# Performance work log

Measured on AMD Instinct MI355X. Metric: run time of the kernel, lower is better.

## Reference

```python
import jax, jax.numpy as jnp
import numpy as np

TOP_K = 8
SCORE_FUNC = "sigmoid"
ROUTE_NORM = True
ROUTE_SCALE = 2.5


def setup_inputs() -> dict:
    key = jax.random.key(0)
    k1, k2, k3 = jax.random.split(key, 3)
    B, S, H, E = 4, 4096, 2048, 64
    hidden_states = jax.random.normal(k1, (B, S, H), dtype=jnp.float32)
    # nn.Linear default init scale ~ 1/sqrt(H); exact distribution irrelevant for correctness
    gate_w = jax.random.normal(k2, (E, H), dtype=jnp.float32) * (1.0 / np.sqrt(H))
    expert_bias = jax.random.normal(k3, (E,), dtype=jnp.float32) * 0.1
    return {"hidden_states": hidden_states, "expert_bias": expert_bias, "gate_w": gate_w}


def reference(hidden_states, expert_bias, gate_w):
    B, S, H = hidden_states.shape
    x = hidden_states.reshape(-1, H)  # [T, H]
    logits = jnp.einsum("th,eh->te", x, gate_w)  # [T, E]
    if SCORE_FUNC == "sigmoid":
        scores = jax.nn.sigmoid(logits.astype(jnp.float32))
    else:
        scores = jax.nn.softmax(logits.astype(jnp.float32), axis=-1)
    if expert_bias is not None:
        _, selected_experts = jax.lax.top_k(scores + expert_bias[None, :], TOP_K)
        top_scores = jnp.take_along_axis(scores, selected_experts, axis=1)
    else:
        top_scores, selected_experts = jax.lax.top_k(scores, TOP_K)
    if SCORE_FUNC == "sigmoid" and ROUTE_NORM:
        denom = jnp.sum(top_scores, axis=-1, keepdims=True) + 1e-20
        top_scores = top_scores / denom
    top_scores = top_scores * ROUTE_SCALE
    return top_scores, selected_experts
```

## Files before the change

kernel.cpp:

```cpp
#include <hip/hip_runtime.h>
#include <math.h>

#define T_TOTAL 16384
#define HDIM    2048
#define NEXP    64
#define KS_MAIN 8

typedef unsigned short ushort_t;
using bf16x8 = __attribute__((ext_vector_type(8))) short;
using f32x4  = __attribute__((ext_vector_type(4))) float;

__device__ __forceinline__ unsigned bf16rne(float f) {
    const unsigned u = __float_as_uint(f);
    return (u + 0x7FFFu + ((u >> 16) & 1u)) >> 16;
}
__device__ __forceinline__ float bf16tof(unsigned b) {
    return __uint_as_float(b << 16);
}

__device__ __forceinline__ void split8(const float4 a, const float4 b,
                                       bf16x8& h, bf16x8& m, bf16x8& l) {
    float f[8] = {a.x, a.y, a.z, a.w, b.x, b.y, b.z, b.w};
    unsigned hb[8], mb[8], lb[8];
#pragma unroll
    for (int j = 0; j < 8; ++j) {
        const float    x  = f[j];
        const unsigned hu = bf16rne(x);
        const float    r1 = x - bf16tof(hu);
        const unsigned mu = bf16rne(r1);
        const float    r2 = r1 - bf16tof(mu);
        const unsigned lu = bf16rne(r2);
        hb[j] = hu; mb[j] = mu; lb[j] = lu;
    }
    union { unsigned u[4]; bf16x8 v; } H, M, L;
#pragma unroll
    for (int d = 0; d < 4; ++d) {
        H.u[d] = hb[2*d] | (hb[2*d+1] << 16);
        M.u[d] = mb[2*d] | (mb[2*d+1] << 16);
        L.u[d] = lb[2*d] | (lb[2*d+1] << 16);
    }
    h = H.v; m = M.v; l = L.v;
}

__global__ void convert_w_kernel(const float* __restrict__ w,
                                 ushort_t* __restrict__ whi,
                                 ushort_t* __restrict__ wmid,
                                 ushort_t* __restrict__ wlo)
{
    const int i = (blockIdx.x * 256 + threadIdx.x) * 4;
    const float4 v = *(const float4*)(w + i);
    float f[4] = {v.x, v.y, v.z, v.w};
#pragma unroll
    for (int j = 0; j < 4; ++j) {
        const float    x  = f[j];
        const unsigned hu = bf16rne(x);
        const float    r1 = x - bf16tof(hu);
        const unsigned mu = bf16rne(r1);
        const float    r2 = r1 - bf16tof(mu);
        const unsigned lu = bf16rne(r2);
        whi [i + j] = (ushort_t)hu;
        wmid[i + j] = (ushort_t)mu;
        wlo [i + j] = (ushort_t)lu;
    }
}

__global__ __launch_bounds__(256, 4)
void router_gemm_mfma(const float*   __restrict__ x,
                      const ushort_t* __restrict__ whi,
                      const ushort_t* __restrict__ wmid,
                      const ushort_t* __restrict__ wlo,
                      float* __restrict__ partial)
{
    constexpr int KSLICE = HDIM / KS_MAIN;
    const int tid  = threadIdx.x;
    const int wv   = tid >> 6;
    const int lane = tid & 63;
    const int tb   = blockIdx.x >> 3;
    const int ks   = blockIdx.x & 7;
    const int t0   = tb * 128 + wv * 32;
    const int k0   = ks * KSLICE;
    const int lr   = lane & 15;
    const int lg   = lane >> 4;
    const int kl   = lg * 8;

    f32x4 acc[2][4];
#pragma unroll
    for (int mt = 0; mt < 2; ++mt)
#pragma unroll
        for (int nt = 0; nt < 4; ++nt) {
            f32x4 z = {0.0f, 0.0f, 0.0f, 0.0f};
            acc[mt][nt] = z;
        }

    const float* px0 = x + (size_t)(t0 + lr) * HDIM + k0 + kl;
    const float* px1 = px0 + (size_t)16 * HDIM;

    const size_t boff = (size_t)lr * HDIM + k0 + kl;
    const ushort_t* pbh = whi  + boff;
    const ushort_t* pbm = wmid + boff;
    const ushort_t* pbl = wlo  + boff;

    float4 c00 = *(const float4*)(px0);
    float4 c01 = *(const float4*)(px0 + 4);
    float4 c10 = *(const float4*)(px1);
    float4 c11 = *(const float4*)(px1 + 4);

#pragma unroll 1
    for (int kk = 0; kk < KSLICE; kk += 32) {
        bf16x8 Ah[2], Am[2], Al[2];
        split8(c00, c01, Ah[0], Am[0], Al[0]);
        split8(c10, c11, Ah[1], Am[1], Al[1]);

        if (kk + 32 < KSLICE) {
            c00 = *(const float4*)(px0 + kk + 32);
            c01 = *(const float4*)(px0 + kk + 36);
            c10 = *(const float4*)(px1 + kk + 32);
            c11 = *(const float4*)(px1 + kk + 36);
        }

#pragma unroll
        for (int nt = 0; nt < 4; ++nt) {
            const size_t no = (size_t)nt * 16 * HDIM + kk;
            const bf16x8 Bh = *(const bf16x8*)(pbh + no);
            const bf16x8 Bm = *(const bf16x8*)(pbm + no);
            const bf16x8 Bl = *(const bf16x8*)(pbl + no);
#pragma unroll
            for (int mt = 0; mt < 2; ++mt) {
                acc[mt][nt] = __builtin_amdgcn_mfma_f32_16x16x32_bf16(Ah[mt], Bh, acc[mt][nt], 0, 0, 0);
                acc[mt][nt] = __builtin_amdgcn_mfma_f32_16x16x32_bf16(Am[mt], Bh, acc[mt][nt], 0, 0, 0);
                acc[mt][nt] = __builtin_amdgcn_mfma_f32_16x16x32_bf16(Al[mt], Bh, acc[mt][nt], 0, 0, 0);
                acc[mt][nt] = __builtin_amdgcn_mfma_f32_16x16x32_bf16(Ah[mt], Bm, acc[mt][nt], 0, 0, 0);
                acc[mt][nt] = __builtin_amdgcn_mfma_f32_16x16x32_bf16(Am[mt], Bm, acc[mt][nt], 0, 0, 0);
                acc[mt][nt] = __builtin_amdgcn_mfma_f32_16x16x32_bf16(Ah[mt], Bl, acc[mt][nt], 0, 0, 0);
            }
        }
    }

#pragma unroll
    for (int mt = 0; mt < 2; ++mt) {
        const int trow = t0 + mt * 16 + lg * 4;
#pragma unroll
        for (int nt = 0; nt < 4; ++nt) {
            float* pb = partial + ((size_t)trow * KS_MAIN + ks) * NEXP + nt * 16 + lr;
#pragma unroll
            for (int r = 0; r < 4; ++r)
                pb[(size_t)r * KS_MAIN * NEXP] = acc[mt][nt][r];
        }
    }
}

__global__ void router_gemm_naive(const float* __restrict__ x,
                                  const float* __restrict__ w,
                                  float* __restrict__ partial)
{
    const int t = blockIdx.x;
    const int e = threadIdx.x;
    const float* xp = x + (size_t)t * HDIM;
    const float* wp = w + (size_t)e * HDIM;
    float s = 0.0f;
    for (int k = 0; k < HDIM; ++k) s = fmaf(xp[k], wp[k], s);
    partial[(size_t)t * NEXP + e] = s;
}

template<int KS>
__global__ __launch_bounds__(256)
void router_topk_kernel(const float* __restrict__ partial,
                        const float* __restrict__ bias,
                        float* __restrict__ out_scores,
                        float* __restrict__ out_idx)
{
    const int token = blockIdx.x * 4 + (threadIdx.x >> 6);
    const int lane  = threadIdx.x & 63;

    const float* pt = partial + (size_t)token * KS * NEXP + lane;
    float logit = 0.0f;
#pragma unroll
    for (int s = 0; s < KS; ++s) logit += pt[(size_t)s * NEXP];

    const float score = 1.0f / (1.0f + expf(-logit));
    float key = score + bias[lane];

    float myscore = 0.0f;
    int   myidx   = 0;
    float denom   = 0.0f;

#pragma unroll
    for (int r = 0; r < 8; ++r) {
        float bk = key;
        int   bi = lane;
#pragma unroll
        for (int off = 32; off > 0; off >>= 1) {
            const float ok = __shfl_xor(bk, off);
            const int   oi = __shfl_xor(bi, off);
            if (ok > bk || (ok == bk && oi < bi)) { bk = ok; bi = oi; }
        }
        const float wsc = __shfl(score, bi);
        denom += wsc;
        if (lane == r)  { myscore = wsc; myidx = bi; }
        if (lane == bi) key = -__builtin_inff();
    }

    const float factor = 2.5f / (denom + 1e-20f);
    if (lane < 8) {
        out_scores[(size_t)token * 8 + lane] = myscore * factor;
        out_idx  [(size_t)token * 8 + lane] = (float)myidx;
    }
}

extern "C" void kernel_launch(void* const* d_in, const int* in_sizes, int n_in,
                              void* d_out, int out_size, void* d_ws, size_t ws_size,
                              hipStream_t stream)
{
    const float* x    = (const float*)d_in[0];
    const float* bias = (const float*)d_in[1];
    const float* w    = (const float*)d_in[2];

    float* out     = (float*)d_out;
    float* partial = (float*)d_ws;

    const size_t partialBytes = (size_t)T_TOTAL * KS_MAIN * NEXP * 4;
    const size_t wplaneElems  = (size_t)NEXP * HDIM;
    const size_t needBytes    = partialBytes + 3 * wplaneElems * sizeof(ushort_t);

    if (ws_size >= needBytes) {
        ushort_t* whi  = (ushort_t*)((char*)d_ws + partialBytes);
        ushort_t* wmid = whi  + wplaneElems;
        ushort_t* wlo  = wmid + wplaneElems;

        convert_w_kernel<<<dim3(128), dim3(256), 0, stream>>>(w, whi, wmid, wlo);
        router_gemm_mfma<<<dim3(128 * KS_MAIN), dim3(256), 0, stream>>>(
            x, whi, wmid, wlo, partial);
        router_topk_kernel<KS_MAIN><<<dim3(T_TOTAL / 4), dim3(256), 0, stream>>>(
            partial, bias, out, out + (size_t)T_TOTAL * 8);
    } else {
        router_gemm_naive<<<dim3(T_TOTAL), dim3(64), 0, stream>>>(x, w, partial);
        router_topk_kernel<1><<<dim3(T_TOTAL / 4), dim3(256), 0, stream>>>(
            partial, bias, out, out + (size_t)T_TOTAL * 8);
    }
}
```

Before: 246.6 us.

## Prefetch B fragments, use packed bf16 convert, simplify top-k argmax via ballot

The split of fp32 activations into three bf16 parts now uses the hardware v_cvt_pk_bf16_f32 instruction, which converts two values at once, in place of manual integer rounding. The weight fragments are software-pipelined: the loads for the next expert tile or k-step are issued before the MFMAs on the current tile, so load latency is hidden behind compute. In the top-k kernel, the index shuffle in each butterfly step is dropped: a max-only reduction is followed by a ballot and find-first-set to pick the lowest matching lane. The prefetch raises register pressure, and at the last k-step it issues a redundant wrap-around load.

```diff
diff --git a/kernel.cpp b/kernel.cpp
--- a/kernel.cpp
+++ b/kernel.cpp
@@ -18,26 +18,28 @@
     return __uint_as_float(b << 16);
 }
 
+__device__ __forceinline__ unsigned cvtpk_bf16(float a, float b) {
+    unsigned r;
+    asm("v_cvt_pk_bf16_f32 %0, %1, %2" : "=v"(r) : "v"(a), "v"(b));
+    return r;
+}
+
 __device__ __forceinline__ void split8(const float4 a, const float4 b,
                                        bf16x8& h, bf16x8& m, bf16x8& l) {
-    float f[8] = {a.x, a.y, a.z, a.w, b.x, b.y, b.z, b.w};
-    unsigned hb[8], mb[8], lb[8];
-#pragma unroll
-    for (int j = 0; j < 8; ++j) {
-        const float    x  = f[j];
-        const unsigned hu = bf16rne(x);
-        const float    r1 = x - bf16tof(hu);
-        const unsigned mu = bf16rne(r1);
-        const float    r2 = r1 - bf16tof(mu);
-        const unsigned lu = bf16rne(r2);
-        hb[j] = hu; mb[j] = mu; lb[j] = lu;
-    }
+    const float f[8] = {a.x, a.y, a.z, a.w, b.x, b.y, b.z, b.w};
     union { unsigned u[4]; bf16x8 v; } H, M, L;
 #pragma unroll
     for (int d = 0; d < 4; ++d) {
-        H.u[d] = hb[2*d] | (hb[2*d+1] << 16);
-        M.u[d] = mb[2*d] | (mb[2*d+1] << 16);
-        L.u[d] = lb[2*d] | (lb[2*d+1] << 16);
+        const float f0 = f[2*d], f1 = f[2*d+1];
+        const unsigned ph = cvtpk_bf16(f0, f1);
+        const float r0 = f0 - __uint_as_float(ph << 16);
+        const float r1 = f1 - __uint_as_float(ph & 0xFFFF0000u);
+        const unsigned pm = cvtpk_bf16(r0, r1);
+        const float s0 = r0 - __uint_as_float(pm << 16);
+        const float s1 = r1 - __uint_as_float(pm & 0xFFFF0000u);
+        H.u[d] = ph;
+        M.u[d] = pm;
+        L.u[d] = cvtpk_bf16(s0, s1);
     }
     h = H.v; m = M.v; l = L.v;
 }
@@ -105,6 +107,10 @@
     float4 c10 = *(const float4*)(px1);
     float4 c11 = *(const float4*)(px1 + 4);
 
+    bf16x8 Bh_c = *(const bf16x8*)(pbh);
+    bf16x8 Bm_c = *(const bf16x8*)(pbm);
+    bf16x8 Bl_c = *(const bf16x8*)(pbl);
+
 #pragma unroll 1
     for (int kk = 0; kk < KSLICE; kk += 32) {
         bf16x8 Ah[2], Am[2], Al[2];
@@ -120,19 +126,25 @@
 
 #pragma unroll
         for (int nt = 0; nt < 4; ++nt) {
-            const size_t no = (size_t)nt * 16 * HDIM + kk;
-            const bf16x8 Bh = *(const bf16x8*)(pbh + no);
-            const bf16x8 Bm = *(const bf16x8*)(pbm + no);
-            const bf16x8 Bl = *(const bf16x8*)(pbl + no);
+            const int ntn = (nt + 1) & 3;
+            int kkn = (nt == 3) ? kk + 32 : kk;
+            if (kkn >= KSLICE) kkn = 0;
+            const size_t non = (size_t)ntn * 16 * HDIM + kkn;
+            bf16x8 Bh_n = *(const bf16x8*)(pbh + non);
+            bf16x8 Bm_n = *(const bf16x8*)(pbm + non);
+            bf16x8 Bl_n = *(const bf16x8*)(pbl + non);
+
 #pragma unroll
             for (int mt = 0; mt < 2; ++mt) {
-                acc[mt][nt] = __builtin_amdgcn_mfma_f32_16x16x32_bf16(Ah[mt], Bh, acc[mt][nt], 0, 0, 0);
-                acc[mt][nt] = __builtin_amdgcn_mfma_f32_16x16x32_bf16(Am[mt], Bh, acc[mt][nt], 0, 0, 0);
-                acc[mt][nt] = __builtin_amdgcn_mfma_f32_16x16x32_bf16(Al[mt], Bh, acc[mt][nt], 0, 0, 0);
-                acc[mt][nt] = __builtin_amdgcn_mfma_f32_16x16x32_bf16(Ah[mt], Bm, acc[mt][nt], 0, 0, 0);
-                acc[mt][nt] = __builtin_amdgcn_mfma_f32_16x16x32_bf16(Am[mt], Bm, acc[mt][nt], 0, 0, 0);
-                acc[mt][nt] = __builtin_amdgcn_mfma_f32_16x16x32_bf16(Ah[mt], Bl, acc[mt][nt], 0, 0, 0);
+                acc[mt][nt] = __builtin_amdgcn_mfma_f32_16x16x32_bf16(Ah[mt], Bh_c, acc[mt][nt], 0, 0, 0);
+                acc[mt][nt] = __builtin_amdgcn_mfma_f32_16x16x32_bf16(Am[mt], Bh_c, acc[mt][nt], 0, 0, 0);
+                acc[mt][nt] = __builtin_amdgcn_mfma_f32_16x16x32_bf16(Al[mt], Bh_c, acc[mt][nt], 0, 0, 0);
+                acc[mt][nt] = __builtin_amdgcn_mfma_f32_16x16x32_bf16(Ah[mt], Bm_c, acc[mt][nt], 0, 0, 0);
+                acc[mt][nt] = __builtin_amdgcn_mfma_f32_16x16x32_bf16(Am[mt], Bm_c, acc[mt][nt], 0, 0, 0);
+                acc[mt][nt] = __builtin_amdgcn_mfma_f32_16x16x32_bf16(Ah[mt], Bl_c, acc[mt][nt], 0, 0, 0);
             }
+
+            Bh_c = Bh_n; Bm_c = Bm_n; Bl_c = Bl_n;
         }
     }
 
@@ -187,13 +199,11 @@
 #pragma unroll
     for (int r = 0; r < 8; ++r) {
         float bk = key;
-        int   bi = lane;
-#pragma unroll
-        for (int off = 32; off > 0; off >>= 1) {
-            const float ok = __shfl_xor(bk, off);
-            const int   oi = __shfl_xor(bi, off);
-            if (ok > bk || (ok == bk && oi < bi)) { bk = ok; bi = oi; }
-        }
+#pragma unroll
+        for (int off = 32; off > 0; off >>= 1)
+            bk = fmaxf(bk, __shfl_xor(bk, off));
+        const unsigned long long msk = __ballot(key == bk);
+        const int bi = __ffsll(msk) - 1;
         const float wsc = __shfl(score, bi);
         denom += wsc;
         if (lane == r)  { myscore = wsc; myidx = bi; }
```

Measured after the change: 233.8 us. 5.2% less time.
